# Kernel tuning notes

Measured on AMD Instinct MI355X. Metric: run time of the kernel, lower is better.

Reference implementation:

```python
import jax, jax.numpy as jnp
import numpy as np
from jax import lax

N_WORDS = 8192
MAX_WLEN = 16
VOCAB = 500
EMB = 64
HID = 256
N_SENT = 256
SENT_LEN = 32  # N_SENT * SENT_LEN == N_WORDS (sentlens are uniform)


def setup_inputs() -> dict:
    key = jax.random.key(0)
    ks = jax.random.split(key, 12)
    chars = jax.random.randint(ks[0], (N_WORDS, MAX_WLEN), 1, VOCAB, dtype=jnp.int32)
    # packed LSTM requires lengths sorted descending
    wordlens = jnp.sort(jax.random.randint(ks[1], (N_WORDS,), 1, MAX_WLEN + 1, dtype=jnp.int32))[::-1]
    # permutation mapping sorted order -> original order (tensor_unsort input)
    word_orig_idx = jax.random.permutation(ks[2], N_WORDS).astype(jnp.int32)
    emb_table = (jax.random.normal(ks[3], (VOCAB, EMB), dtype=jnp.float32) * 0.1).at[0].set(0.0)  # padding_idx=0
    W_ih = jax.random.normal(ks[4], (4 * HID, EMB), dtype=jnp.float32) * 0.05
    W_hh = jax.random.normal(ks[5], (4 * HID, HID), dtype=jnp.float32) * 0.05
    b_ih = jax.random.normal(ks[6], (4 * HID,), dtype=jnp.float32) * 0.02
    b_hh = jax.random.normal(ks[7], (4 * HID,), dtype=jnp.float32) * 0.02
    attn_w = jax.random.normal(ks[8], (HID,), dtype=jnp.float32) * 0.1  # char_attn weight (zero-init in orig; random for nontrivial test)
    h_init = jax.random.normal(ks[9], (HID,), dtype=jnp.float32) * 0.02  # charlstm_h_init (num_layers=1)
    c_init = jax.random.normal(ks[10], (HID,), dtype=jnp.float32) * 0.02
    return dict(chars=chars, wordlens=wordlens, word_orig_idx=word_orig_idx,
                emb_table=emb_table, W_ih=W_ih, W_hh=W_hh, b_ih=b_ih, b_hh=b_hh,
                attn_w=attn_w, h_init=h_init, c_init=c_init)


def _char_model(chars, wordlens, word_orig_idx, emb_table, W_ih, W_hh, b_ih, b_hh, attn_w, h_init, c_init):
    n = chars.shape[0]
    pad_mask = jnp.arange(MAX_WLEN)[None, :] >= wordlens[:, None]  # [N,L] True where padded
    embs = emb_table[chars]  # [N,L,E] (dropout is identity at eval)

    def step(carry, x_t):
        h, c = carry
        gates = x_t @ W_ih.T + h @ W_hh.T + (b_ih + b_hh)  # [N,4H]
        i, f, g, o = jnp.split(gates, 4, axis=-1)  # torch gate order i,f,g,o
        c = jax.nn.sigmoid(f) * c + jax.nn.sigmoid(i) * jnp.tanh(g)
        h = jax.nn.sigmoid(o) * jnp.tanh(c)
        return (h, c), h

    h0 = jnp.broadcast_to(h_init, (n, HID))
    c0 = jnp.broadcast_to(c_init, (n, HID))
    _, hs = lax.scan(step, (h0, c0), embs.transpose(1, 0, 2))  # hs: [L,N,H]
    char_reps = hs.transpose(1, 0, 2)  # [N,L,H]
    # pad_packed_sequence yields zeros at padded positions
    char_reps = jnp.where(pad_mask[..., None], 0.0, char_reps)
    # masked sigmoid attention pool: weights.bmm(char_reps)
    w = jax.nn.sigmoid(char_reps @ attn_w)  # [N,L]
    w = jnp.where(pad_mask, 0.0, w)
    res = jnp.einsum('nl,nlh->nh', w, char_reps)  # [N,H]
    # tensor_unsort: restore original word order
    res = jnp.zeros_like(res).at[word_orig_idx].set(res)
    # split(sentlens) + pack + pad_packed with uniform sentlens -> reshape
    return res.reshape(N_SENT, SENT_LEN, HID)


def reference(chars, wordlens, word_orig_idx, emb_table, W_ih, W_hh, b_ih, b_hh, attn_w, h_init, c_init):
    return _char_model(chars, wordlens, word_orig_idx, emb_table, W_ih, W_hh, b_ih, b_hh, attn_w, h_init, c_init)
```

## Files before the change

kernel.cpp:

```cpp
#include <hip/hip_runtime.h>
#include <math.h>

#define HID 256
#define EMB 64
#define KTOT 320
#define MT 32
#define NBLK 256
#define THREADS 512
#define KT 10
#define XSTR 328

typedef _Float16 f16;
typedef _Float16 f16x4 __attribute__((ext_vector_type(4)));
typedef _Float16 f16x8 __attribute__((ext_vector_type(8)));
typedef float f32x4 __attribute__((ext_vector_type(4)));

__device__ __forceinline__ float sigm(float x) { return 1.0f / (1.0f + __expf(-x)); }

__global__ __launch_bounds__(KTOT) void prep_w(const float* __restrict__ W_ih,
                                               const float* __restrict__ W_hh,
                                               const float* __restrict__ b_ih,
                                               const float* __restrict__ b_hh,
                                               f16* __restrict__ Wfrag,
                                               float* __restrict__ bias_p) {
  const int g = blockIdx.x;
  const int k = threadIdx.x;
  const int q = g >> 8, u = g & 255;
  const int col = ((u >> 5) << 7) + (q << 5) + (((u >> 4) & 1) << 4) + (u & 15);
  const float w = (k < HID) ? W_hh[g * HID + k] : W_ih[g * EMB + (k - HID)];
  const int kt = k >> 5;
  Wfrag[((size_t)(kt * 1024 + col)) * 32 + (k & 31)] = (f16)w;
  if (k == 0) bias_p[col] = b_ih[g] + b_hh[g];
}

__global__ __launch_bounds__(THREADS, 2) void lstm_mfma(
    const int* __restrict__ chars, const int* __restrict__ wordlens,
    const int* __restrict__ orig_idx, const float* __restrict__ emb_table,
    const float* __restrict__ attn_w, const float* __restrict__ h_init,
    const float* __restrict__ c_init, const f16* __restrict__ Wfrag,
    const float* __restrict__ bias_p, float* __restrict__ out) {
  __shared__ __align__(16) f16 Xs[MT * XSTR];
  __shared__ __align__(16) float attP[MT * 8];
  __shared__ int chars_s[MT * 16];
  __shared__ int len_s[MT];
  __shared__ int oidx_s[MT];

  const int tid  = threadIdx.x;
  const int w0   = blockIdx.x * MT;
  const int lane = tid & 63;
  const int wv   = tid >> 6;
  const int r15  = lane & 15, c4 = lane >> 4;
  const int u0   = wv * 32 + r15;

  chars_s[tid] = chars[w0 * 16 + tid];
  if (tid < MT) { len_s[tid] = wordlens[w0 + tid]; oidx_s[tid] = orig_idx[w0 + tid]; }

  {
    const int j = tid & 255, mb = tid >> 8;
    const f16 hv = (f16)h_init[j];
#pragma unroll
    for (int mm = 0; mm < 16; ++mm) Xs[(mb + mm * 2) * XSTR + j] = hv;
  }
  {
    const int m = tid >> 4, e4 = tid & 15;
    const int ch_g = chars[(w0 + m) * 16 + 0];
    const float4 e = ((const float4*)emb_table)[ch_g * 16 + e4];
    f16x4 ev = { (f16)e.x, (f16)e.y, (f16)e.z, (f16)e.w };
    *(f16x4*)&Xs[m * XSTR + HID + e4 * 4] = ev;
  }

  const float aw0 = attn_w[u0];
  const float aw1 = attn_w[u0 + 16];
  float biasr[4][2];
#pragma unroll
  for (int q = 0; q < 4; ++q) {
    biasr[q][0] = bias_p[wv * 128 + q * 32 + r15];
    biasr[q][1] = bias_p[wv * 128 + q * 32 + 16 + r15];
  }

  float c_reg[2][8], res[2][8], h_new[2][8];
  {
    const float c0 = c_init[u0], c1 = c_init[u0 + 16];
#pragma unroll
    for (int i = 0; i < 8; ++i) {
      c_reg[0][i] = c0; c_reg[1][i] = c1;
      res[0][i] = 0.0f; res[1][i] = 0.0f;
      h_new[0][i] = 0.0f; h_new[1][i] = 0.0f;
    }
  }

  __syncthreads();

  int steps = 1;
#pragma unroll
  for (int m = 0; m < MT; ++m) steps = max(steps, len_s[m]);
  int lenr[8];
#pragma unroll
  for (int mt = 0; mt < 2; ++mt)
#pragma unroll
    for (int r = 0; r < 4; ++r) lenr[mt * 4 + r] = len_s[mt * 16 + c4 * 4 + r];

  const size_t bofs = (size_t)(wv * 128 + r15) * 4 + c4;

  for (int t = 0; t < steps; ++t) {
    f32x4 acc[4][2][2];
#pragma unroll
    for (int q = 0; q < 4; ++q)
#pragma unroll
      for (int s = 0; s < 2; ++s) {
        const float b = biasr[q][s];
        const f32x4 b4 = { b, b, b, b };
        acc[q][s][0] = b4; acc[q][s][1] = b4;
      }

#pragma unroll 2
    for (int kt = 0; kt < KT; ++kt) {
      const f16x8* __restrict__ Wp = ((const f16x8*)Wfrag) + (size_t)kt * 4096;
      const f16x8 a0 = *(const f16x8*)&Xs[r15 * XSTR + kt * 32 + c4 * 8];
      const f16x8 a1 = *(const f16x8*)&Xs[(16 + r15) * XSTR + kt * 32 + c4 * 8];
#pragma unroll
      for (int q = 0; q < 4; ++q) {
#pragma unroll
        for (int s = 0; s < 2; ++s) {
          const f16x8 b = Wp[bofs + (size_t)(q * 32 + s * 16) * 4];
          acc[q][s][0] = __builtin_amdgcn_mfma_f32_16x16x32_f16(a0, b, acc[q][s][0], 0, 0, 0);
          acc[q][s][1] = __builtin_amdgcn_mfma_f32_16x16x32_f16(a1, b, acc[q][s][1], 0, 0, 0);
        }
      }
    }

#pragma unroll
    for (int s = 0; s < 2; ++s)
#pragma unroll
      for (int mt = 0; mt < 2; ++mt)
#pragma unroll
        for (int r = 0; r < 4; ++r) {
          const int i = mt * 4 + r;
          const float gi = acc[0][s][mt][r];
          const float gf = acc[1][s][mt][r];
          const float gg = acc[2][s][mt][r];
          const float go = acc[3][s][mt][r];
          const float cc = sigm(gf) * c_reg[s][i] + sigm(gi) * tanhf(gg);
          c_reg[s][i] = cc;
          h_new[s][i] = sigm(go) * tanhf(cc);
        }

    __syncthreads();

    if (t + 1 < steps) {
#pragma unroll
      for (int s = 0; s < 2; ++s)
#pragma unroll
        for (int mt = 0; mt < 2; ++mt)
#pragma unroll
          for (int r = 0; r < 4; ++r)
            Xs[(mt * 16 + c4 * 4 + r) * XSTR + u0 + s * 16] = (f16)h_new[s][mt * 4 + r];
      {
        const int m = tid >> 4, e4 = tid & 15;
        const int ch = chars_s[m * 16 + (t + 1)];
        const float4 e = ((const float4*)emb_table)[ch * 16 + e4];
        f16x4 ev = { (f16)e.x, (f16)e.y, (f16)e.z, (f16)e.w };
        *(f16x4*)&Xs[m * XSTR + HID + e4 * 4] = ev;
      }
    }

#pragma unroll
    for (int mt = 0; mt < 2; ++mt)
#pragma unroll
      for (int r = 0; r < 4; ++r) {
        const int i = mt * 4 + r;
        float p = h_new[0][i] * aw0 + h_new[1][i] * aw1;
        p += __shfl_xor(p, 1); p += __shfl_xor(p, 2);
        p += __shfl_xor(p, 4); p += __shfl_xor(p, 8);
        if (r15 == 0) attP[(mt * 16 + c4 * 4 + r) * 8 + wv] = p;
      }

    __syncthreads();

#pragma unroll
    for (int mt = 0; mt < 2; ++mt)
#pragma unroll
      for (int r = 0; r < 4; ++r) {
        const int i = mt * 4 + r;
        const int w = mt * 16 + c4 * 4 + r;
        const f32x4 p0 = *(const f32x4*)&attP[w * 8];
        const f32x4 p1 = *(const f32x4*)&attP[w * 8 + 4];
        const float sum = (p0[0] + p0[1]) + (p0[2] + p0[3]) + (p1[0] + p1[1]) + (p1[2] + p1[3]);
        const float wgt = (t < lenr[i]) ? sigm(sum) : 0.0f;
        res[0][i] = fmaf(wgt, h_new[0][i], res[0][i]);
        res[1][i] = fmaf(wgt, h_new[1][i], res[1][i]);
      }
  }

#pragma unroll
  for (int s = 0; s < 2; ++s)
#pragma unroll
    for (int mt = 0; mt < 2; ++mt)
#pragma unroll
      for (int r = 0; r < 4; ++r) {
        const int w = mt * 16 + c4 * 4 + r;
        out[(size_t)oidx_s[w] * HID + u0 + s * 16] = res[s][mt * 4 + r];
      }
}

extern "C" void kernel_launch(void* const* d_in, const int* in_sizes, int n_in,
                              void* d_out, int out_size, void* d_ws, size_t ws_size,
                              hipStream_t stream) {
  const int*   chars    = (const int*)d_in[0];
  const int*   wordlens = (const int*)d_in[1];
  const int*   orig_idx = (const int*)d_in[2];
  const float* emb      = (const float*)d_in[3];
  const float* W_ih     = (const float*)d_in[4];
  const float* W_hh     = (const float*)d_in[5];
  const float* b_ih     = (const float*)d_in[6];
  const float* b_hh     = (const float*)d_in[7];
  const float* attn_w   = (const float*)d_in[8];
  const float* h_init   = (const float*)d_in[9];
  const float* c_init   = (const float*)d_in[10];
  float* out = (float*)d_out;

  f16*   Wfrag  = (f16*)d_ws;
  float* bias_p = (float*)((char*)d_ws + (size_t)KTOT * 1024 * sizeof(f16));
  if (ws_size < (size_t)KTOT * 1024 * sizeof(f16) + 1024 * sizeof(float)) return;

  hipLaunchKernelGGL(prep_w, dim3(1024), dim3(KTOT), 0, stream,
                     W_ih, W_hh, b_ih, b_hh, Wfrag, bias_p);
  hipLaunchKernelGGL(lstm_mfma, dim3(NBLK), dim3(THREADS), 0, stream,
                     chars, wordlens, orig_idx, emb, attn_w, h_init, c_init,
                     Wfrag, bias_p, out);
}
```

Baseline: 253.2 us.

## Halve words per block to 16 and use fast exp-based tanh

Each block now processes 16 words instead of 32, which doubles the grid to 512 blocks. Every wave issues half as many MFMAs per step while the weight fragment loads stay the same. The intent is to spread the sequential recurrence over more CUs and cut per-step latency, at the cost of reading the weight stream from L2 twice as often overall. tanhf is also replaced with a cheaper __expf-based formula, which may lose accuracy or overflow for large inputs.

```diff
diff --git a/kernel.cpp b/kernel.cpp
--- a/kernel.cpp
+++ b/kernel.cpp
@@ -4,18 +4,21 @@
 #define HID 256
 #define EMB 64
 #define KTOT 320
-#define MT 32
-#define NBLK 256
+#define MT 16
+#define NBLK 512
 #define THREADS 512
 #define KT 10
 #define XSTR 328
 
 typedef _Float16 f16;
-typedef _Float16 f16x4 __attribute__((ext_vector_type(4)));
+typedef _Float16 f16x2 __attribute__((ext_vector_type(2)));
 typedef _Float16 f16x8 __attribute__((ext_vector_type(8)));
 typedef float f32x4 __attribute__((ext_vector_type(4)));
 
 __device__ __forceinline__ float sigm(float x) { return 1.0f / (1.0f + __expf(-x)); }
+__device__ __forceinline__ float tanh_fast(float x) {
+  return 1.0f - 2.0f / (__expf(2.0f * x) + 1.0f);
+}
 
 __global__ __launch_bounds__(KTOT) void prep_w(const float* __restrict__ W_ih,
                                                const float* __restrict__ W_hh,
@@ -52,21 +55,21 @@
   const int r15  = lane & 15, c4 = lane >> 4;
   const int u0   = wv * 32 + r15;
 
-  chars_s[tid] = chars[w0 * 16 + tid];
+  if (tid < MT * 16) chars_s[tid] = chars[w0 * 16 + tid];
   if (tid < MT) { len_s[tid] = wordlens[w0 + tid]; oidx_s[tid] = orig_idx[w0 + tid]; }
 
   {
     const int j = tid & 255, mb = tid >> 8;
     const f16 hv = (f16)h_init[j];
 #pragma unroll
-    for (int mm = 0; mm < 16; ++mm) Xs[(mb + mm * 2) * XSTR + j] = hv;
+    for (int mm = 0; mm < 8; ++mm) Xs[(mb + mm * 2) * XSTR + j] = hv;
   }
   {
-    const int m = tid >> 4, e4 = tid & 15;
+    const int m = tid >> 5, e2 = tid & 31;
     const int ch_g = chars[(w0 + m) * 16 + 0];
-    const float4 e = ((const float4*)emb_table)[ch_g * 16 + e4];
-    f16x4 ev = { (f16)e.x, (f16)e.y, (f16)e.z, (f16)e.w };
-    *(f16x4*)&Xs[m * XSTR + HID + e4 * 4] = ev;
+    const float2 e = ((const float2*)emb_table)[ch_g * 32 + e2];
+    f16x2 ev = { (f16)e.x, (f16)e.y };
+    *(f16x2*)&Xs[m * XSTR + HID + e2 * 2] = ev;
   }
 
   const float aw0 = attn_w[u0];
@@ -78,11 +81,11 @@
     biasr[q][1] = bias_p[wv * 128 + q * 32 + 16 + r15];
   }
 
-  float c_reg[2][8], res[2][8], h_new[2][8];
+  float c_reg[2][4], res[2][4], h_new[2][4];
   {
     const float c0 = c_init[u0], c1 = c_init[u0 + 16];
 #pragma unroll
-    for (int i = 0; i < 8; ++i) {
+    for (int i = 0; i < 4; ++i) {
       c_reg[0][i] = c0; c_reg[1][i] = c1;
       res[0][i] = 0.0f; res[1][i] = 0.0f;
       h_new[0][i] = 0.0f; h_new[1][i] = 0.0f;
@@ -94,56 +97,48 @@
   int steps = 1;
 #pragma unroll
   for (int m = 0; m < MT; ++m) steps = max(steps, len_s[m]);
-  int lenr[8];
-#pragma unroll
-  for (int mt = 0; mt < 2; ++mt)
-#pragma unroll
-    for (int r = 0; r < 4; ++r) lenr[mt * 4 + r] = len_s[mt * 16 + c4 * 4 + r];
+  int lenr[4];
+#pragma unroll
+  for (int r = 0; r < 4; ++r) lenr[r] = len_s[c4 * 4 + r];
 
   const size_t bofs = (size_t)(wv * 128 + r15) * 4 + c4;
 
   for (int t = 0; t < steps; ++t) {
-    f32x4 acc[4][2][2];
+    f32x4 acc[4][2];
 #pragma unroll
     for (int q = 0; q < 4; ++q)
 #pragma unroll
       for (int s = 0; s < 2; ++s) {
         const float b = biasr[q][s];
         const f32x4 b4 = { b, b, b, b };
-        acc[q][s][0] = b4; acc[q][s][1] = b4;
+        acc[q][s] = b4;
       }
 
 #pragma unroll 2
     for (int kt = 0; kt < KT; ++kt) {
       const f16x8* __restrict__ Wp = ((const f16x8*)Wfrag) + (size_t)kt * 4096;
       const f16x8 a0 = *(const f16x8*)&Xs[r15 * XSTR + kt * 32 + c4 * 8];
-      const f16x8 a1 = *(const f16x8*)&Xs[(16 + r15) * XSTR + kt * 32 + c4 * 8];
-#pragma unroll
-      for (int q = 0; q < 4; ++q) {
+#pragma unroll
+      for (int q = 0; q < 4; ++q)
 #pragma unroll
         for (int s = 0; s < 2; ++s) {
           const f16x8 b = Wp[bofs + (size_t)(q * 32 + s * 16) * 4];
-          acc[q][s][0] = __builtin_amdgcn_mfma_f32_16x16x32_f16(a0, b, acc[q][s][0], 0, 0, 0);
-          acc[q][s][1] = __builtin_amdgcn_mfma_f32_16x16x32_f16(a1, b, acc[q][s][1], 0, 0, 0);
+          acc[q][s] = __builtin_amdgcn_mfma_f32_16x16x32_f16(a0, b, acc[q][s], 0, 0, 0);
         }
+    }
+
+#pragma unroll
+    for (int s = 0; s < 2; ++s)
+#pragma unroll
+      for (int r = 0; r < 4; ++r) {
+        const float gi = acc[0][s][r];
+        const float gf = acc[1][s][r];
+        const float gg = acc[2][s][r];
+        const float go = acc[3][s][r];
+        const float cc = sigm(gf) * c_reg[s][r] + sigm(gi) * tanh_fast(gg);
+        c_reg[s][r] = cc;
+        h_new[s][r] = sigm(go) * tanh_fast(cc);
       }
-    }
-
-#pragma unroll
-    for (int s = 0; s < 2; ++s)
-#pragma unroll
-      for (int mt = 0; mt < 2; ++mt)
-#pragma unroll
-        for (int r = 0; r < 4; ++r) {
-          const int i = mt * 4 + r;
-          const float gi = acc[0][s][mt][r];
-          const float gf = acc[1][s][mt][r];
-          const float gg = acc[2][s][mt][r];
-          const float go = acc[3][s][mt][r];
-          const float cc = sigm(gf) * c_reg[s][i] + sigm(gi) * tanhf(gg);
-          c_reg[s][i] = cc;
-          h_new[s][i] = sigm(go) * tanhf(cc);
-        }
 
     __syncthreads();
 
@@ -151,56 +146,46 @@
 #pragma unroll
       for (int s = 0; s < 2; ++s)
 #pragma unroll
-        for (int mt = 0; mt < 2; ++mt)
-#pragma unroll
-          for (int r = 0; r < 4; ++r)
-            Xs[(mt * 16 + c4 * 4 + r) * XSTR + u0 + s * 16] = (f16)h_new[s][mt * 4 + r];
+        for (int r = 0; r < 4; ++r)
+          Xs[(c4 * 4 + r) * XSTR + u0 + s * 16] = (f16)h_new[s][r];
       {
-        const int m = tid >> 4, e4 = tid & 15;
+        const int m = tid >> 5, e2 = tid & 31;
         const int ch = chars_s[m * 16 + (t + 1)];
-        const float4 e = ((const float4*)emb_table)[ch * 16 + e4];
-        f16x4 ev = { (f16)e.x, (f16)e.y, (f16)e.z, (f16)e.w };
-        *(f16x4*)&Xs[m * XSTR + HID + e4 * 4] = ev;
+        const float2 e = ((const float2*)emb_table)[ch * 32 + e2];
+        f16x2 ev = { (f16)e.x, (f16)e.y };
+        *(f16x2*)&Xs[m * XSTR + HID + e2 * 2] = ev;
       }
     }
 
 #pragma unroll
-    for (int mt = 0; mt < 2; ++mt)
-#pragma unroll
-      for (int r = 0; r < 4; ++r) {
-        const int i = mt * 4 + r;
-        float p = h_new[0][i] * aw0 + h_new[1][i] * aw1;
-        p += __shfl_xor(p, 1); p += __shfl_xor(p, 2);
-        p += __shfl_xor(p, 4); p += __shfl_xor(p, 8);
-        if (r15 == 0) attP[(mt * 16 + c4 * 4 + r) * 8 + wv] = p;
-      }
+    for (int r = 0; r < 4; ++r) {
+      float p = h_new[0][r] * aw0 + h_new[1][r] * aw1;
+      p += __shfl_xor(p, 1); p += __shfl_xor(p, 2);
+      p += __shfl_xor(p, 4); p += __shfl_xor(p, 8);
+      if (r15 == 0) attP[(c4 * 4 + r) * 8 + wv] = p;
+    }
 
     __syncthreads();
 
 #pragma unroll
-    for (int mt = 0; mt < 2; ++mt)
-#pragma unroll
-      for (int r = 0; r < 4; ++r) {
-        const int i = mt * 4 + r;
-        const int w = mt * 16 + c4 * 4 + r;
-        const f32x4 p0 = *(const f32x4*)&attP[w * 8];
-        const f32x4 p1 = *(const f32x4*)&attP[w * 8 + 4];
-        const float sum = (p0[0] + p0[1]) + (p0[2] + p0[3]) + (p1[0] + p1[1]) + (p1[2] + p1[3]);
-        const float wgt = (t < lenr[i]) ? sigm(sum) : 0.0f;
-        res[0][i] = fmaf(wgt, h_new[0][i], res[0][i]);
-        res[1][i] = fmaf(wgt, h_new[1][i], res[1][i]);
-      }
+    for (int r = 0; r < 4; ++r) {
+      const int w = c4 * 4 + r;
+      const f32x4 p0 = *(const f32x4*)&attP[w * 8];
+      const f32x4 p1 = *(const f32x4*)&attP[w * 8 + 4];
+      const float sum = (p0[0] + p0[1]) + (p0[2] + p0[3]) + (p1[0] + p1[1]) + (p1[2] + p1[3]);
+      const float wgt = (t < lenr[r]) ? sigm(sum) : 0.0f;
+      res[0][r] = fmaf(wgt, h_new[0][r], res[0][r]);
+      res[1][r] = fmaf(wgt, h_new[1][r], res[1][r]);
+    }
   }
 
 #pragma unroll
   for (int s = 0; s < 2; ++s)
 #pragma unroll
-    for (int mt = 0; mt < 2; ++mt)
-#pragma unroll
-      for (int r = 0; r < 4; ++r) {
-        const int w = mt * 16 + c4 * 4 + r;
-        out[(size_t)oidx_s[w] * HID + u0 + s * 16] = res[s][mt * 4 + r];
-      }
+    for (int r = 0; r < 4; ++r) {
+      const int w = c4 * 4 + r;
+      out[(size_t)oidx_s[w] * HID + u0 + s * 16] = res[s][r];
+    }
 }
 
 extern "C" void kernel_launch(void* const* d_in, const int* in_sizes, int n_in,
```

Result: slower. 263.8 us (+4.2%).

## Stream weight tiles into double-buffered LDS via async global-to-LDS loads

Applied to the files above, without the earlier changes.

Weights are re-laid out per wave and k-tile so each wave can stream its slice into a two-slot LDS ring with global_load_lds. The next-next k-tile is prefetched while MFMAs run on the current one, and waits on vmcnt replace per-kt global loads from L2. Other changes: the next step's embedding is prefetched before the GEMM, tanhf is replaced with an exp-based tanh, and __syncthreads becomes a lighter LDS-only barrier. Costs are 128KB of LDS per block, which likely drops occupancy to one block per CU, and hand-written waitcnt counts that must stay correct.

```diff
diff --git a/kernel.cpp b/kernel.cpp
--- a/kernel.cpp
+++ b/kernel.cpp
@@ -16,29 +16,43 @@
 typedef float f32x4 __attribute__((ext_vector_type(4)));
 
 __device__ __forceinline__ float sigm(float x) { return 1.0f / (1.0f + __expf(-x)); }
+__device__ __forceinline__ float tanh_fast(float x) {
+  return 1.0f - 2.0f / (__expf(2.0f * x) + 1.0f);
+}
+
+__device__ __forceinline__ void bar_lds() {
+  asm volatile("s_waitcnt lgkmcnt(0)" ::: "memory");
+  __builtin_amdgcn_sched_barrier(0);
+  __builtin_amdgcn_s_barrier();
+  __builtin_amdgcn_sched_barrier(0);
+}
 
 __global__ __launch_bounds__(KTOT) void prep_w(const float* __restrict__ W_ih,
                                                const float* __restrict__ W_hh,
                                                const float* __restrict__ b_ih,
                                                const float* __restrict__ b_hh,
-                                               f16* __restrict__ Wfrag,
+                                               f16* __restrict__ Wfrag2,
                                                float* __restrict__ bias_p) {
   const int g = blockIdx.x;
   const int k = threadIdx.x;
   const int q = g >> 8, u = g & 255;
-  const int col = ((u >> 5) << 7) + (q << 5) + (((u >> 4) & 1) << 4) + (u & 15);
+  const int wv  = u >> 5;
+  const int f   = q * 2 + ((u >> 4) & 1);
+  const int r15 = u & 15;
+  const int kt = k >> 5, c4 = (k >> 3) & 3, e = k & 7;
+  const int lane = c4 * 16 + r15;
   const float w = (k < HID) ? W_hh[g * HID + k] : W_ih[g * EMB + (k - HID)];
-  const int kt = k >> 5;
-  Wfrag[((size_t)(kt * 1024 + col)) * 32 + (k & 31)] = (f16)w;
-  if (k == 0) bias_p[col] = b_ih[g] + b_hh[g];
+  Wfrag2[(size_t)kt * 32768 + wv * 4096 + f * 512 + lane * 8 + e] = (f16)w;
+  if (k == 0) bias_p[wv * 128 + f * 16 + r15] = b_ih[g] + b_hh[g];
 }
 
 __global__ __launch_bounds__(THREADS, 2) void lstm_mfma(
     const int* __restrict__ chars, const int* __restrict__ wordlens,
     const int* __restrict__ orig_idx, const float* __restrict__ emb_table,
     const float* __restrict__ attn_w, const float* __restrict__ h_init,
-    const float* __restrict__ c_init, const f16* __restrict__ Wfrag,
+    const float* __restrict__ c_init, const f16* __restrict__ Wfrag2,
     const float* __restrict__ bias_p, float* __restrict__ out) {
+  __shared__ __align__(16) f16 Bs[2][32768];
   __shared__ __align__(16) f16 Xs[MT * XSTR];
   __shared__ __align__(16) float attP[MT * 8];
   __shared__ int chars_s[MT * 16];
@@ -74,8 +88,8 @@
   float biasr[4][2];
 #pragma unroll
   for (int q = 0; q < 4; ++q) {
-    biasr[q][0] = bias_p[wv * 128 + q * 32 + r15];
-    biasr[q][1] = bias_p[wv * 128 + q * 32 + 16 + r15];
+    biasr[q][0] = bias_p[wv * 128 + (q * 2 + 0) * 16 + r15];
+    biasr[q][1] = bias_p[wv * 128 + (q * 2 + 1) * 16 + r15];
   }
 
   float c_reg[2][8], res[2][8], h_new[2][8];
@@ -89,6 +103,20 @@
     }
   }
 
+  const f16* __restrict__ srcW = Wfrag2 + (size_t)wv * 4096 + lane * 8;
+#pragma unroll
+  for (int i = 0; i < 8; ++i)
+    __builtin_amdgcn_global_load_lds(
+        (const __attribute__((address_space(1))) unsigned int*)(srcW + 0 * 32768 + i * 512),
+        (__attribute__((address_space(3))) unsigned int*)(&Bs[0][wv * 4096 + i * 512]),
+        16, 0, 0);
+#pragma unroll
+  for (int i = 0; i < 8; ++i)
+    __builtin_amdgcn_global_load_lds(
+        (const __attribute__((address_space(1))) unsigned int*)(srcW + 1 * 32768 + i * 512),
+        (__attribute__((address_space(3))) unsigned int*)(&Bs[1][wv * 4096 + i * 512]),
+        16, 0, 0);
+
   __syncthreads();
 
   int steps = 1;
@@ -100,54 +128,81 @@
 #pragma unroll
     for (int r = 0; r < 4; ++r) lenr[mt * 4 + r] = len_s[mt * 16 + c4 * 4 + r];
 
-  const size_t bofs = (size_t)(wv * 128 + r15) * 4 + c4;
-
   for (int t = 0; t < steps; ++t) {
-    f32x4 acc[4][2][2];
+    float4 embnx;
+    const bool have_nx = (t + 1 < steps);
+    if (have_nx) {
+      const int m = tid >> 4, e4 = tid & 15;
+      const int ch = chars_s[m * 16 + (t + 1)];
+      embnx = ((const float4*)emb_table)[ch * 16 + e4];
+    }
+
+    f32x4 acc[4][2];
+    f32x4 acc2[4][2];
 #pragma unroll
     for (int q = 0; q < 4; ++q)
 #pragma unroll
       for (int s = 0; s < 2; ++s) {
         const float b = biasr[q][s];
         const f32x4 b4 = { b, b, b, b };
-        acc[q][s][0] = b4; acc[q][s][1] = b4;
-      }
-
-#pragma unroll 2
+        acc[q][s] = b4; acc2[q][s] = b4;
+      }
+
+#pragma unroll
     for (int kt = 0; kt < KT; ++kt) {
-      const f16x8* __restrict__ Wp = ((const f16x8*)Wfrag) + (size_t)kt * 4096;
+      asm volatile("s_waitcnt vmcnt(8)" ::: "memory");
+      __builtin_amdgcn_sched_barrier(0);
+
+      const f16* __restrict__ bsl = &Bs[kt & 1][wv * 4096 + lane * 8];
+      f16x8 bb[8];
+#pragma unroll
+      for (int f = 0; f < 8; ++f) bb[f] = *(const f16x8*)(bsl + f * 512);
       const f16x8 a0 = *(const f16x8*)&Xs[r15 * XSTR + kt * 32 + c4 * 8];
       const f16x8 a1 = *(const f16x8*)&Xs[(16 + r15) * XSTR + kt * 32 + c4 * 8];
-#pragma unroll
-      for (int q = 0; q < 4; ++q) {
+
+      asm volatile("s_waitcnt lgkmcnt(0)" ::: "memory");
+      __builtin_amdgcn_sched_barrier(0);
+
+      {
+        const int ktn = (kt + 2 < KT) ? (kt + 2) : (kt + 2 - KT);
+        const f16* __restrict__ s2 = srcW + (size_t)ktn * 32768;
+#pragma unroll
+        for (int i = 0; i < 8; ++i)
+          __builtin_amdgcn_global_load_lds(
+              (const __attribute__((address_space(1))) unsigned int*)(s2 + i * 512),
+              (__attribute__((address_space(3))) unsigned int*)(&Bs[kt & 1][wv * 4096 + i * 512]),
+              16, 0, 0);
+      }
+
+#pragma unroll
+      for (int q = 0; q < 4; ++q)
 #pragma unroll
         for (int s = 0; s < 2; ++s) {
-          const f16x8 b = Wp[bofs + (size_t)(q * 32 + s * 16) * 4];
-          acc[q][s][0] = __builtin_amdgcn_mfma_f32_16x16x32_f16(a0, b, acc[q][s][0], 0, 0, 0);
-          acc[q][s][1] = __builtin_amdgcn_mfma_f32_16x16x32_f16(a1, b, acc[q][s][1], 0, 0, 0);
+          acc[q][s]  = __builtin_amdgcn_mfma_f32_16x16x32_f16(a0, bb[q * 2 + s], acc[q][s],  0, 0, 0);
+          acc2[q][s] = __builtin_amdgcn_mfma_f32_16x16x32_f16(a1, bb[q * 2 + s], acc2[q][s], 0, 0, 0);
         }
-      }
     }
 
 #pragma unroll
     for (int s = 0; s < 2; ++s)
 #pragma unroll
-      for (int mt = 0; mt < 2; ++mt)
-#pragma unroll
-        for (int r = 0; r < 4; ++r) {
-          const int i = mt * 4 + r;
-          const float gi = acc[0][s][mt][r];
-          const float gf = acc[1][s][mt][r];
-          const float gg = acc[2][s][mt][r];
-          const float go = acc[3][s][mt][r];
-          const float cc = sigm(gf) * c_reg[s][i] + sigm(gi) * tanhf(gg);
+      for (int r = 0; r < 4; ++r) {
+        {
+          const float cc = sigm(acc[1][s][r]) * c_reg[s][r] + sigm(acc[0][s][r]) * tanh_fast(acc[2][s][r]);
+          c_reg[s][r] = cc;
+          h_new[s][r] = sigm(acc[3][s][r]) * tanh_fast(cc);
+        }
+        {
+          const int i = 4 + r;
+          const float cc = sigm(acc2[1][s][r]) * c_reg[s][i] + sigm(acc2[0][s][r]) * tanh_fast(acc2[2][s][r]);
           c_reg[s][i] = cc;
-          h_new[s][i] = sigm(go) * tanhf(cc);
+          h_new[s][i] = sigm(acc2[3][s][r]) * tanh_fast(cc);
         }
-
-    __syncthreads();
-
-    if (t + 1 < steps) {
+      }
+
+    bar_lds();
+
+    if (have_nx) {
 #pragma unroll
       for (int s = 0; s < 2; ++s)
 #pragma unroll
@@ -157,9 +212,7 @@
             Xs[(mt * 16 + c4 * 4 + r) * XSTR + u0 + s * 16] = (f16)h_new[s][mt * 4 + r];
       {
         const int m = tid >> 4, e4 = tid & 15;
-        const int ch = chars_s[m * 16 + (t + 1)];
-        const float4 e = ((const float4*)emb_table)[ch * 16 + e4];
-        f16x4 ev = { (f16)e.x, (f16)e.y, (f16)e.z, (f16)e.w };
+        f16x4 ev = { (f16)embnx.x, (f16)embnx.y, (f16)embnx.z, (f16)embnx.w };
         *(f16x4*)&Xs[m * XSTR + HID + e4 * 4] = ev;
       }
     }
@@ -175,7 +228,7 @@
         if (r15 == 0) attP[(mt * 16 + c4 * 4 + r) * 8 + wv] = p;
       }
 
-    __syncthreads();
+    bar_lds();
 
 #pragma unroll
     for (int mt = 0; mt < 2; ++mt)
@@ -219,13 +272,13 @@
   const float* c_init   = (const float*)d_in[10];
   float* out = (float*)d_out;
 
-  f16*   Wfrag  = (f16*)d_ws;
-  float* bias_p = (float*)((char*)d_ws + (size_t)KTOT * 1024 * sizeof(f16));
-  if (ws_size < (size_t)KTOT * 1024 * sizeof(f16) + 1024 * sizeof(float)) return;
+  f16*   Wfrag2 = (f16*)d_ws;
+  float* bias_p = (float*)((char*)d_ws + (size_t)KT * 32768 * sizeof(f16));
+  if (ws_size < (size_t)KT * 32768 * sizeof(f16) + 1024 * sizeof(float)) return;
 
   hipLaunchKernelGGL(prep_w, dim3(1024), dim3(KTOT), 0, stream,
-                     W_ih, W_hh, b_ih, b_hh, Wfrag, bias_p);
+                     W_ih, W_hh, b_ih, b_hh, Wfrag2, bias_p);
   hipLaunchKernelGGL(lstm_mfma, dim3(NBLK), dim3(THREADS), 0, stream,
                      chars, wordlens, orig_idx, emb, attn_w, h_init, c_init,
-                     Wfrag, bias_p, out);
-}
+                     Wfrag2, bias_p, out);
+}
```

New measurement: 400.7 us. 58.2% more time.

## Software-pipeline weight fragment loads in registers and use fast exp-based tanh

Applied to the files above, without the earlier changes.

Weight fragments for the MFMA K-loop are now prefetched two k-tiles ahead into a double-buffered register array, with the loop fully unrolled and wrapping around across timesteps. The intent is to hide global/L2 load latency behind the MFMAs. Occupancy drops from 2 blocks to 1 per CU, giving the compiler more registers for the prefetch buffers. tanhf is also replaced with an exp-based formula, which is cheaper but slightly less accurate and can lose precision near zero.

```diff
diff --git a/kernel.cpp b/kernel.cpp
--- a/kernel.cpp
+++ b/kernel.cpp
@@ -16,6 +16,9 @@
 typedef float f32x4 __attribute__((ext_vector_type(4)));
 
 __device__ __forceinline__ float sigm(float x) { return 1.0f / (1.0f + __expf(-x)); }
+__device__ __forceinline__ float tanh_fast(float x) {
+  return 1.0f - 2.0f / (__expf(2.0f * x) + 1.0f);
+}
 
 __global__ __launch_bounds__(KTOT) void prep_w(const float* __restrict__ W_ih,
                                                const float* __restrict__ W_hh,
@@ -33,7 +36,8 @@
   if (k == 0) bias_p[col] = b_ih[g] + b_hh[g];
 }
 
-__global__ __launch_bounds__(THREADS, 2) void lstm_mfma(
+__global__ __launch_bounds__(THREADS, 1)
+void lstm_mfma(
     const int* __restrict__ chars, const int* __restrict__ wordlens,
     const int* __restrict__ orig_idx, const float* __restrict__ emb_table,
     const float* __restrict__ attn_w, const float* __restrict__ h_init,
@@ -89,6 +93,15 @@
     }
   }
 
+  const size_t bofs = (size_t)(wv * 128 + r15) * 4 + c4;
+  const f16x8* __restrict__ Wp8 = (const f16x8*)Wfrag;
+
+  f16x8 bb[2][8];
+#pragma unroll
+  for (int f = 0; f < 8; ++f) bb[0][f] = Wp8[(size_t)0 * 4096 + bofs + (size_t)f * 64];
+#pragma unroll
+  for (int f = 0; f < 8; ++f) bb[1][f] = Wp8[(size_t)1 * 4096 + bofs + (size_t)f * 64];
+
   __syncthreads();
 
   int steps = 1;
@@ -99,8 +112,6 @@
   for (int mt = 0; mt < 2; ++mt)
 #pragma unroll
     for (int r = 0; r < 4; ++r) lenr[mt * 4 + r] = len_s[mt * 16 + c4 * 4 + r];
-
-  const size_t bofs = (size_t)(wv * 128 + r15) * 4 + c4;
 
   for (int t = 0; t < steps; ++t) {
     f32x4 acc[4][2][2];
@@ -113,19 +124,23 @@
         acc[q][s][0] = b4; acc[q][s][1] = b4;
       }
 
-#pragma unroll 2
+#pragma unroll
     for (int kt = 0; kt < KT; ++kt) {
-      const f16x8* __restrict__ Wp = ((const f16x8*)Wfrag) + (size_t)kt * 4096;
+      const int slot = kt & 1;
       const f16x8 a0 = *(const f16x8*)&Xs[r15 * XSTR + kt * 32 + c4 * 8];
       const f16x8 a1 = *(const f16x8*)&Xs[(16 + r15) * XSTR + kt * 32 + c4 * 8];
 #pragma unroll
-      for (int q = 0; q < 4; ++q) {
+      for (int q = 0; q < 4; ++q)
 #pragma unroll
         for (int s = 0; s < 2; ++s) {
-          const f16x8 b = Wp[bofs + (size_t)(q * 32 + s * 16) * 4];
-          acc[q][s][0] = __builtin_amdgcn_mfma_f32_16x16x32_f16(a0, b, acc[q][s][0], 0, 0, 0);
-          acc[q][s][1] = __builtin_amdgcn_mfma_f32_16x16x32_f16(a1, b, acc[q][s][1], 0, 0, 0);
+          acc[q][s][0] = __builtin_amdgcn_mfma_f32_16x16x32_f16(a0, bb[slot][q * 2 + s], acc[q][s][0], 0, 0, 0);
+          acc[q][s][1] = __builtin_amdgcn_mfma_f32_16x16x32_f16(a1, bb[slot][q * 2 + s], acc[q][s][1], 0, 0, 0);
         }
+      {
+        const int ktn = (kt + 2 < KT) ? (kt + 2) : (kt + 2 - KT);
+        const f16x8* __restrict__ Wn = Wp8 + (size_t)ktn * 4096;
+#pragma unroll
+        for (int f = 0; f < 8; ++f) bb[slot][f] = Wn[bofs + (size_t)f * 64];
       }
     }
 
@@ -140,9 +155,9 @@
           const float gf = acc[1][s][mt][r];
           const float gg = acc[2][s][mt][r];
           const float go = acc[3][s][mt][r];
-          const float cc = sigm(gf) * c_reg[s][i] + sigm(gi) * tanhf(gg);
+          const float cc = sigm(gf) * c_reg[s][i] + sigm(gi) * tanh_fast(gg);
           c_reg[s][i] = cc;
-          h_new[s][i] = sigm(go) * tanhf(cc);
+          h_new[s][i] = sigm(go) * tanh_fast(cc);
         }
 
     __syncthreads();
```

Result: slower. 391.2 us (+54.5%).
